# Kernel optimization log

Hardware: AMD Instinct MI355X
Metric: run time of the kernel (lower is better)

## Reference

```python
import jax, jax.numpy as jnp
import numpy as np

B, S, D = 4, 2048, 1024
H, DK, DV = 16, 64, 64
EPS = 1e-5


def setup_inputs() -> dict:
    key = jax.random.key(0)
    ks = jax.random.split(key, 12)
    sc = 0.02
    return {
        "q": jax.random.normal(ks[0], (B, S, D), jnp.float32),
        "k": jax.random.normal(ks[1], (B, S, D), jnp.float32),
        "v": jax.random.normal(ks[2], (B, S, D), jnp.float32),
        "Wq": jax.random.normal(ks[3], (D, H * DK), jnp.float32) * sc,
        "bq": jnp.zeros((H * DK,), jnp.float32),
        "Wk": jax.random.normal(ks[4], (D, H * DK), jnp.float32) * sc,
        "bk": jnp.zeros((H * DK,), jnp.float32),
        "Wv": jax.random.normal(ks[5], (D, H * DV), jnp.float32) * sc,
        "bv": jnp.zeros((H * DV,), jnp.float32),
        "Wfc": jax.random.normal(ks[6], (H * DV, D), jnp.float32) * sc,
        "bfc": jnp.zeros((D,), jnp.float32),
        "gamma": jnp.ones((D,), jnp.float32),
        "beta": jnp.zeros((D,), jnp.float32),
    }


def _forward(q, k, v, Wq, bq, Wk, bk, Wv, bv, Wfc, bfc, gamma, beta):
    qp = q @ Wq + bq                      # [B,S,H*DK]
    kp = k @ Wk + bk
    vp = v @ Wv + bv
    qh = qp.reshape(B, S, H, DK).transpose(0, 2, 1, 3)  # [B,H,S,DK]
    kh = kp.reshape(B, S, H, DK).transpose(0, 2, 1, 3)
    vh = vp.reshape(B, S, H, DV).transpose(0, 2, 1, 3)
    scores = jnp.einsum("bhqd,bhkd->bhqk", qh, kh) / jnp.sqrt(jnp.float32(DK))
    attn = jax.nn.softmax(scores, axis=-1)
    ctx = jnp.einsum("bhqk,bhkd->bhqd", attn, vh)       # [B,H,S,DV]
    ctx = ctx.transpose(0, 2, 1, 3).reshape(B, S, H * DV)
    out = ctx @ Wfc + bfc                 # [B,S,D]
    residual = qp                         # n_heads*d_k == d_model
    x = out + residual
    mu = jnp.mean(x, axis=-1, keepdims=True)
    var = jnp.mean((x - mu) ** 2, axis=-1, keepdims=True)
    return (x - mu) / jnp.sqrt(var + EPS) * gamma + beta


def reference(q, k, v, Wq, bq, Wk, bk, Wv, bv, Wfc, bfc, gamma, beta):
    return _forward(q, k, v, Wq, bq, Wk, bk, Wv, bv, Wfc, bfc, gamma, beta)
```

## Files before the change

### kernel.cpp

```cpp
#include <hip/hip_runtime.h>
#include <hip/hip_bf16.h>
#include <stdint.h>

typedef __bf16 bf16x8 __attribute__((ext_vector_type(8)));
typedef __bf16 bf16x4 __attribute__((ext_vector_type(4)));
typedef short  s16x4  __attribute__((ext_vector_type(4)));
typedef float  f32x4  __attribute__((ext_vector_type(4)));

#define MFMA_K32(a,b,c) __builtin_amdgcn_mfma_f32_16x16x32_bf16((a),(b),(c),0,0,0)

__device__ __forceinline__ f32x4 pv_mfma(s16x4 a, s16x4 b, f32x4 c) {
#if defined(__HIP_DEVICE_COMPILE__)
    return __builtin_amdgcn_mfma_f32_16x16x16bf16_1k(a, b, c, 0, 0, 0);
#else
    return c;
#endif
}

__device__ __forceinline__ void gld16(const void* g, void* l) {
#if defined(__HIP_DEVICE_COMPILE__)
    __builtin_amdgcn_global_load_lds((__attribute__((address_space(1))) void*)(g),
                                     (__attribute__((address_space(3))) void*)(l), 16, 0, 0);
#endif
}

#define CS 0.180336880111f

__global__ __launch_bounds__(256) void cast3_kernel(const float* __restrict__ q,
                                                    const float* __restrict__ k,
                                                    const float* __restrict__ v,
                                                    __hip_bfloat16* __restrict__ qb,
                                                    __hip_bfloat16* __restrict__ kb,
                                                    __hip_bfloat16* __restrict__ vb) {
    const float* x = (blockIdx.y == 0) ? q : (blockIdx.y == 1) ? k : v;
    __hip_bfloat16* y = (blockIdx.y == 0) ? qb : (blockIdx.y == 1) ? kb : vb;
    int i = blockIdx.x * 256 + threadIdx.x;
    float4 vv = ((const float4*)x)[i];
    union { ushort4 u; __hip_bfloat16 b[4]; } c;
    c.b[0] = __float2bfloat16(vv.x);
    c.b[1] = __float2bfloat16(vv.y);
    c.b[2] = __float2bfloat16(vv.z);
    c.b[3] = __float2bfloat16(vv.w);
    ((ushort4*)y)[i] = c.u;
}

__global__ __launch_bounds__(256) void transpose_w_kernel(const float* __restrict__ Wq,
                                                          const float* __restrict__ Wk,
                                                          const float* __restrict__ Wv,
                                                          const float* __restrict__ Wfc,
                                                          __hip_bfloat16* __restrict__ WqT,
                                                          __hip_bfloat16* __restrict__ WkT,
                                                          __hip_bfloat16* __restrict__ WvT,
                                                          __hip_bfloat16* __restrict__ WfcT) {
    int z = blockIdx.z;
    const float* W = (z == 0) ? Wq : (z == 1) ? Wk : (z == 2) ? Wv : Wfc;
    __hip_bfloat16* Wt = (z == 0) ? WqT : (z == 1) ? WkT : (z == 2) ? WvT : WfcT;
    __shared__ float tile[32][33];
    int n0 = blockIdx.x * 32, k0 = blockIdx.y * 32;
    int tx = threadIdx.x & 31, ty = threadIdx.x >> 5;
    for (int i = ty; i < 32; i += 8)
        tile[i][tx] = W[(size_t)(k0 + i) * 1024 + n0 + tx];
    __syncthreads();
    for (int i = ty; i < 32; i += 8)
        Wt[(size_t)(n0 + i) * 1024 + k0 + tx] = __float2bfloat16(tile[tx][i]);
}

__global__ __launch_bounds__(256) void transpose_v_kernel(const __hip_bfloat16* __restrict__ vp,
                                                          __hip_bfloat16* __restrict__ vt) {
    __shared__ __hip_bfloat16 tile[64][65];
    int s0 = blockIdx.x * 64;
    int bh = blockIdx.y; int bb = bh >> 4, h = bh & 15;
    int tx = threadIdx.x & 63, ty = threadIdx.x >> 6;
    for (int i = ty; i < 64; i += 4)
        tile[i][tx] = vp[(size_t)(bb * 2048 + s0 + i) * 1024 + h * 64 + tx];
    __syncthreads();
    for (int i = ty; i < 64; i += 4)
        vt[((size_t)bh * 64 + i) * 2048 + s0 + tx] = tile[tx][i];
}

__global__ __launch_bounds__(256) void gemm_qkv_kernel(const __hip_bfloat16* __restrict__ qb,
                                                       const __hip_bfloat16* __restrict__ kb,
                                                       const __hip_bfloat16* __restrict__ vb,
                                                       const __hip_bfloat16* __restrict__ WqT,
                                                       const __hip_bfloat16* __restrict__ WkT,
                                                       const __hip_bfloat16* __restrict__ WvT,
                                                       const float* __restrict__ bq,
                                                       const float* __restrict__ bk,
                                                       const float* __restrict__ bv,
                                                       __hip_bfloat16* __restrict__ qp,
                                                       __hip_bfloat16* __restrict__ kp,
                                                       __hip_bfloat16* __restrict__ vp) {
    __shared__ __attribute__((aligned(16))) __hip_bfloat16 As[2][128 * 32];
    __shared__ __attribute__((aligned(16))) __hip_bfloat16 Bs[2][128 * 32];
    const int t = threadIdx.x;
    const int lane = t & 63, w = t >> 6;
    const int m16 = lane & 15, quad = lane >> 4;
    const int wm = w >> 1, wn = w & 1;
    const int sel = blockIdx.y >> 3;
    const int bn = blockIdx.y & 7, bm = blockIdx.x;

    const __hip_bfloat16* A;  const __hip_bfloat16* Bt;
    const float* bias;        __hip_bfloat16* out;
    float oscale = 1.0f;
    if (sel == 0)      { A = qb; Bt = WqT; bias = bq; out = qp; }
    else if (sel == 1) { A = kb; Bt = WkT; bias = bk; out = kp; oscale = CS; }
    else               { A = vb; Bt = WvT; bias = bv; out = vp; }

    const __hip_bfloat16* Ag = A + (size_t)(bm * 128 + (t >> 2)) * 1024 + (t & 3) * 8;
    const __hip_bfloat16* Bg = Bt + (size_t)(bn * 128 + (t >> 2)) * 1024 + (t & 3) * 8;

    auto stage = [&](int k0, int buf) {
        gld16(Ag + k0,                    &As[buf][t * 8]);
        gld16(Ag + (size_t)64 * 1024 + k0, &As[buf][2048 + t * 8]);
        gld16(Bg + k0,                    &Bs[buf][t * 8]);
        gld16(Bg + (size_t)64 * 1024 + k0, &Bs[buf][2048 + t * 8]);
    };

    f32x4 acc[4][4] = {};
    stage(0, 0);

    for (int k0 = 0; k0 < 1024; k0 += 32) {
        const int buf = (k0 >> 5) & 1;
        __syncthreads();
        if (k0 + 32 < 1024) stage(k0 + 32, buf ^ 1);
        bf16x8 af[4], bfr[4];
#pragma unroll
        for (int i = 0; i < 4; ++i) {
            af[i]  = *(const bf16x8*)&As[buf][(wm * 64 + i * 16 + m16) * 32 + quad * 8];
            bfr[i] = *(const bf16x8*)&Bs[buf][(wn * 64 + i * 16 + m16) * 32 + quad * 8];
        }
#pragma unroll
        for (int i = 0; i < 4; ++i)
#pragma unroll
            for (int j = 0; j < 4; ++j)
                acc[i][j] = MFMA_K32(af[i], bfr[j], acc[i][j]);
    }

#pragma unroll
    for (int j = 0; j < 4; ++j) {
        int col = bn * 128 + wn * 64 + j * 16 + m16;
        float bv_ = bias[col];
#pragma unroll
        for (int i = 0; i < 4; ++i) {
            int row0 = bm * 128 + wm * 64 + i * 16 + quad * 4;
#pragma unroll
            for (int r = 0; r < 4; ++r)
                out[(size_t)(row0 + r) * 1024 + col] = __float2bfloat16((acc[i][j][r] + bv_) * oscale);
        }
    }
}

__global__ __launch_bounds__(256) void gemm_fc_kernel(const __hip_bfloat16* __restrict__ A,
                                                      const __hip_bfloat16* __restrict__ Bt,
                                                      const float* __restrict__ bias,
                                                      const __hip_bfloat16* __restrict__ res,
                                                      float* __restrict__ Cf) {
    __shared__ __attribute__((aligned(16))) __hip_bfloat16 As[2][64 * 32];
    __shared__ __attribute__((aligned(16))) __hip_bfloat16 Bs[2][128 * 32];
    const int t = threadIdx.x;
    const int lane = t & 63, w = t >> 6;
    const int m16 = lane & 15, quad = lane >> 4;
    const int bm = blockIdx.x, bn = blockIdx.y;

    const __hip_bfloat16* Ag = A + (size_t)(bm * 64 + (t >> 2)) * 1024 + (t & 3) * 8;
    const __hip_bfloat16* Bg = Bt + (size_t)(bn * 128 + (t >> 2)) * 1024 + (t & 3) * 8;

    auto stage = [&](int k0, int buf) {
        gld16(Ag + k0,                     &As[buf][t * 8]);
        gld16(Bg + k0,                     &Bs[buf][t * 8]);
        gld16(Bg + (size_t)64 * 1024 + k0, &Bs[buf][2048 + t * 8]);
    };

    f32x4 acc[4][2] = {};
    stage(0, 0);

    for (int k0 = 0; k0 < 1024; k0 += 32) {
        const int buf = (k0 >> 5) & 1;
        __syncthreads();
        if (k0 + 32 < 1024) stage(k0 + 32, buf ^ 1);
        bf16x8 af[4], bfr[2];
#pragma unroll
        for (int i = 0; i < 4; ++i)
            af[i] = *(const bf16x8*)&As[buf][(i * 16 + m16) * 32 + quad * 8];
#pragma unroll
        for (int j = 0; j < 2; ++j)
            bfr[j] = *(const bf16x8*)&Bs[buf][(w * 32 + j * 16 + m16) * 32 + quad * 8];
#pragma unroll
        for (int i = 0; i < 4; ++i)
#pragma unroll
            for (int j = 0; j < 2; ++j)
                acc[i][j] = MFMA_K32(af[i], bfr[j], acc[i][j]);
    }

#pragma unroll
    for (int j = 0; j < 2; ++j) {
        int col = bn * 128 + w * 32 + j * 16 + m16;
        float bv_ = bias[col];
#pragma unroll
        for (int i = 0; i < 4; ++i) {
            int row0 = bm * 64 + i * 16 + quad * 4;
#pragma unroll
            for (int r = 0; r < 4; ++r) {
                size_t idx = (size_t)(row0 + r) * 1024 + col;
                Cf[idx] = acc[i][j][r] + bv_ + __bfloat162float(res[idx]);
            }
        }
    }
}

__global__ __launch_bounds__(256, 2) void attn_kernel(const __hip_bfloat16* __restrict__ qp,
                                                      const __hip_bfloat16* __restrict__ kp,
                                                      const __hip_bfloat16* __restrict__ vt,
                                                      __hip_bfloat16* __restrict__ ctx) {
    __shared__ __attribute__((aligned(16))) __hip_bfloat16 Ks[2][128 * 64];
    __shared__ __attribute__((aligned(16))) __hip_bfloat16 Vs[2][64 * 136];

    const int t = threadIdx.x;
    const int lane = t & 63, w = t >> 6;
    const int m16 = lane & 15, quad = lane >> 4;
    const int qtile = blockIdx.x >> 3;
    const int bh = (blockIdx.x & 7) + 8 * blockIdx.y;
    const int b = bh >> 4, h = bh & 15;

    const __hip_bfloat16* qbase = qp + (size_t)(b * 2048 + qtile * 128 + w * 32) * 1024 + h * 64;
    bf16x8 qf[2][2];
#pragma unroll
    for (int nt = 0; nt < 2; ++nt)
#pragma unroll
        for (int ks = 0; ks < 2; ++ks)
            qf[nt][ks] = *(const bf16x8*)(qbase + (size_t)(nt * 16 + m16) * 1024 + ks * 32 + quad * 8);

    const __hip_bfloat16* kg_ = kp + (size_t)(b * 2048) * 1024 + h * 64;
    const __hip_bfloat16* vg_ = vt + (size_t)bh * 64 * 2048;

    auto stageK = [&](int kt, int buf) {
#pragma unroll
        for (int i = 0; i < 4; ++i) {
            int key = kt * 128 + (i & 1) * 64 + (t >> 2);
            gld16(kg_ + (size_t)key * 1024 + (i >> 1) * 32 + (t & 3) * 8, &Ks[buf][i * 2048 + t * 8]);
        }
    };
    bf16x8 vreg[4];
    auto loadV = [&](int kt) {
#pragma unroll
        for (int i = 0; i < 4; ++i)
            vreg[i] = *(const bf16x8*)(vg_ + (size_t)(i * 16 + (t >> 4)) * 2048 + kt * 128 + (t & 15) * 8);
    };
    auto writeV = [&](int buf) {
#pragma unroll
        for (int i = 0; i < 4; ++i)
            *(bf16x8*)&Vs[buf][(i * 16 + (t >> 4)) * 136 + (t & 15) * 8] = vreg[i];
    };

    f32x4 oacc[4][2] = {};
    f32x4 lsv[2] = {};

    stageK(0, 0);
    loadV(0);

    for (int kt = 0; kt < 16; ++kt) {
        const int buf = kt & 1;
        writeV(buf);
        __syncthreads();
        if (kt + 1 < 16) { stageK(kt + 1, buf ^ 1); loadV(kt + 1); }

        f32x4 sacc[8][2] = {};
#pragma unroll
        for (int ks = 0; ks < 2; ++ks)
#pragma unroll
            for (int mt = 0; mt < 8; ++mt) {
                bf16x8 kf = *(const bf16x8*)&Ks[buf][ks * 4096 + (mt * 16 + m16) * 32 + quad * 8];
                sacc[mt][0] = MFMA_K32(kf, qf[0][ks], sacc[mt][0]);
                sacc[mt][1] = MFMA_K32(kf, qf[1][ks], sacc[mt][1]);
            }

        s16x4 pf[8][2];
#pragma unroll
        for (int mt = 0; mt < 8; ++mt)
#pragma unroll
            for (int nt = 0; nt < 2; ++nt) {
                union { s16x4 s; __bf16 bb[4]; } up;
#pragma unroll
                for (int r = 0; r < 4; ++r) {
                    float pv = __builtin_amdgcn_exp2f(sacc[mt][nt][r]);
                    lsv[nt][r] += pv;
                    up.bb[r] = (__bf16)pv;
                }
                pf[mt][nt] = up.s;
            }

#pragma unroll
        for (int dt = 0; dt < 4; ++dt)
#pragma unroll
            for (int ks2 = 0; ks2 < 8; ++ks2) {
                bf16x4 vfb = *(const bf16x4*)&Vs[buf][(dt * 16 + m16) * 136 + ks2 * 16 + quad * 4];
                s16x4 vf = __builtin_bit_cast(s16x4, vfb);
                oacc[dt][0] = pv_mfma(vf, pf[ks2][0], oacc[dt][0]);
                oacc[dt][1] = pv_mfma(vf, pf[ks2][1], oacc[dt][1]);
            }
    }

    float inv[2];
#pragma unroll
    for (int nt = 0; nt < 2; ++nt) {
        float l = lsv[nt][0] + lsv[nt][1] + lsv[nt][2] + lsv[nt][3];
        l += __shfl_xor(l, 16);
        l += __shfl_xor(l, 32);
        inv[nt] = __builtin_amdgcn_rcpf(l);
    }
#pragma unroll
    for (int nt = 0; nt < 2; ++nt) {
        size_t token = (size_t)b * 2048 + qtile * 128 + w * 32 + nt * 16 + m16;
#pragma unroll
        for (int dt = 0; dt < 4; ++dt) {
            union { bf16x4 v; __bf16 bb[4]; } uo;
#pragma unroll
            for (int r = 0; r < 4; ++r)
                uo.bb[r] = (__bf16)(oacc[dt][nt][r] * inv[nt]);
            *(bf16x4*)(ctx + token * 1024 + h * 64 + dt * 16 + quad * 4) = uo.v;
        }
    }
}

__global__ __launch_bounds__(256) void layernorm_kernel(const float* __restrict__ x,
                                                        const float* __restrict__ gamma,
                                                        const float* __restrict__ beta,
                                                        float* __restrict__ out) {
    int row = blockIdx.x;
    int t = threadIdx.x;
    const float4* xr = (const float4*)(x + (size_t)row * 1024);
    float4 v = xr[t];
    float s  = v.x + v.y + v.z + v.w;
    float s2 = v.x * v.x + v.y * v.y + v.z * v.z + v.w * v.w;
#pragma unroll
    for (int off = 32; off > 0; off >>= 1) {
        s  += __shfl_down(s, off);
        s2 += __shfl_down(s2, off);
    }
    __shared__ float red[8];
    int w = t >> 6, lane = t & 63;
    if (lane == 0) { red[w] = s; red[4 + w] = s2; }
    __syncthreads();
    s  = red[0] + red[1] + red[2] + red[3];
    s2 = red[4] + red[5] + red[6] + red[7];
    float mu  = s * (1.f / 1024.f);
    float var = s2 * (1.f / 1024.f) - mu * mu;
    float rstd = rsqrtf(var + 1e-5f);
    float4 g  = ((const float4*)gamma)[t];
    float4 be = ((const float4*)beta)[t];
    float4 o;
    o.x = (v.x - mu) * rstd * g.x + be.x;
    o.y = (v.y - mu) * rstd * g.y + be.y;
    o.z = (v.z - mu) * rstd * g.z + be.z;
    o.w = (v.w - mu) * rstd * g.w + be.w;
    ((float4*)(out + (size_t)row * 1024))[t] = o;
}

extern "C" void kernel_launch(void* const* d_in, const int* in_sizes, int n_in,
                              void* d_out, int out_size, void* d_ws, size_t ws_size,
                              hipStream_t stream) {
    const float* q    = (const float*)d_in[0];
    const float* k    = (const float*)d_in[1];
    const float* v    = (const float*)d_in[2];
    const float* Wq   = (const float*)d_in[3];
    const float* bq   = (const float*)d_in[4];
    const float* Wk   = (const float*)d_in[5];
    const float* bk   = (const float*)d_in[6];
    const float* Wv   = (const float*)d_in[7];
    const float* bv   = (const float*)d_in[8];
    const float* Wfc  = (const float*)d_in[9];
    const float* bfc  = (const float*)d_in[10];
    const float* gamma= (const float*)d_in[11];
    const float* beta = (const float*)d_in[12];
    float* out = (float*)d_out;

    char* ws = (char*)d_ws;
    const size_t SZ  = (size_t)8192 * 1024 * 2;
    const size_t WSZ = (size_t)1024 * 1024 * 2;
    __hip_bfloat16* qb  = (__hip_bfloat16*)(ws + 0 * SZ);
    __hip_bfloat16* kb  = (__hip_bfloat16*)(ws + 1 * SZ);
    __hip_bfloat16* vb  = (__hip_bfloat16*)(ws + 2 * SZ);
    __hip_bfloat16* qp  = (__hip_bfloat16*)(ws + 3 * SZ);
    __hip_bfloat16* kp  = (__hip_bfloat16*)(ws + 4 * SZ);
    __hip_bfloat16* vp  = (__hip_bfloat16*)(ws + 5 * SZ);
    __hip_bfloat16* ctx = (__hip_bfloat16*)(ws + 6 * SZ);
    __hip_bfloat16* WqT = (__hip_bfloat16*)(ws + 7 * SZ);
    __hip_bfloat16* WkT = (__hip_bfloat16*)(ws + 7 * SZ + 1 * WSZ);
    __hip_bfloat16* WvT = (__hip_bfloat16*)(ws + 7 * SZ + 2 * WSZ);
    __hip_bfloat16* WfcT= (__hip_bfloat16*)(ws + 7 * SZ + 3 * WSZ);
    float*          x   = (float*)(ws + 0 * SZ);
    __hip_bfloat16* vt  = vb;

    cast3_kernel<<<dim3(8192, 3), 256, 0, stream>>>(q, k, v, qb, kb, vb);

    transpose_w_kernel<<<dim3(32, 32, 4), 256, 0, stream>>>(Wq, Wk, Wv, Wfc, WqT, WkT, WvT, WfcT);

    gemm_qkv_kernel<<<dim3(64, 24), 256, 0, stream>>>(qb, kb, vb, WqT, WkT, WvT,
                                                      bq, bk, bv, qp, kp, vp);

    transpose_v_kernel<<<dim3(32, 64), 256, 0, stream>>>(vp, vt);

    attn_kernel<<<dim3(128, 8), 256, 0, stream>>>(qp, kp, vt, ctx);

    gemm_fc_kernel<<<dim3(128, 8), 256, 0, stream>>>(ctx, WfcT, bfc, qp, x);

    layernorm_kernel<<<8192, 256, 0, stream>>>(x, gamma, beta, out);
}
```

Before: 376.0 us.

## Fuse input cast into QKV GEMM, enlarge FC tile, use MFMA for softmax row sums

The separate fp32-to-bf16 cast kernel is removed. The QKV GEMM now loads fp32 activations into registers, packs them to bf16 with a cheap rounding perm and stores them into LDS, overlapping this with the MFMAs. That saves a full write and re-read of three 32 MB tensors. The FC GEMM moves from 64x128 to 128x128 tiles (half the grid). The attention kernel packs P with a faster bf16 conversion, reorders the PV loop, and computes row sums with an extra MFMA against a ones vector instead of scalar adds and shuffles. Costs: register pressure from the held fp32 A tile, and rounding that differs slightly from round-to-nearest-even (no NaN handling).

```diff
diff --git a/kernel.cpp b/kernel.cpp
--- a/kernel.cpp
+++ b/kernel.cpp
@@ -24,25 +24,17 @@
 #endif
 }
 
+__device__ __forceinline__ uint32_t pkbf16(float f0, float f1) {
+    uint32_t u0 = __builtin_bit_cast(uint32_t, f0) + 0x8000u;
+    uint32_t u1 = __builtin_bit_cast(uint32_t, f1) + 0x8000u;
+#if defined(__HIP_DEVICE_COMPILE__)
+    return __builtin_amdgcn_perm(u1, u0, 0x07060302u);
+#else
+    return (u0 >> 16) | (u1 & 0xFFFF0000u);
+#endif
+}
+
 #define CS 0.180336880111f
-
-__global__ __launch_bounds__(256) void cast3_kernel(const float* __restrict__ q,
-                                                    const float* __restrict__ k,
-                                                    const float* __restrict__ v,
-                                                    __hip_bfloat16* __restrict__ qb,
-                                                    __hip_bfloat16* __restrict__ kb,
-                                                    __hip_bfloat16* __restrict__ vb) {
-    const float* x = (blockIdx.y == 0) ? q : (blockIdx.y == 1) ? k : v;
-    __hip_bfloat16* y = (blockIdx.y == 0) ? qb : (blockIdx.y == 1) ? kb : vb;
-    int i = blockIdx.x * 256 + threadIdx.x;
-    float4 vv = ((const float4*)x)[i];
-    union { ushort4 u; __hip_bfloat16 b[4]; } c;
-    c.b[0] = __float2bfloat16(vv.x);
-    c.b[1] = __float2bfloat16(vv.y);
-    c.b[2] = __float2bfloat16(vv.z);
-    c.b[3] = __float2bfloat16(vv.w);
-    ((ushort4*)y)[i] = c.u;
-}
 
 __global__ __launch_bounds__(256) void transpose_w_kernel(const float* __restrict__ Wq,
                                                           const float* __restrict__ Wk,
@@ -78,9 +70,9 @@
         vt[((size_t)bh * 64 + i) * 2048 + s0 + tx] = tile[tx][i];
 }
 
-__global__ __launch_bounds__(256) void gemm_qkv_kernel(const __hip_bfloat16* __restrict__ qb,
-                                                       const __hip_bfloat16* __restrict__ kb,
-                                                       const __hip_bfloat16* __restrict__ vb,
+__global__ __launch_bounds__(256) void gemm_qkv_kernel(const float* __restrict__ q,
+                                                       const float* __restrict__ k,
+                                                       const float* __restrict__ v,
                                                        const __hip_bfloat16* __restrict__ WqT,
                                                        const __hip_bfloat16* __restrict__ WkT,
                                                        const __hip_bfloat16* __restrict__ WvT,
@@ -99,20 +91,96 @@
     const int sel = blockIdx.y >> 3;
     const int bn = blockIdx.y & 7, bm = blockIdx.x;
 
-    const __hip_bfloat16* A;  const __hip_bfloat16* Bt;
-    const float* bias;        __hip_bfloat16* out;
+    const float* A;  const __hip_bfloat16* Bt;
+    const float* bias;  __hip_bfloat16* out;
     float oscale = 1.0f;
-    if (sel == 0)      { A = qb; Bt = WqT; bias = bq; out = qp; }
-    else if (sel == 1) { A = kb; Bt = WkT; bias = bk; out = kp; oscale = CS; }
-    else               { A = vb; Bt = WvT; bias = bv; out = vp; }
+    if (sel == 0)      { A = q; Bt = WqT; bias = bq; out = qp; }
+    else if (sel == 1) { A = k; Bt = WkT; bias = bk; out = kp; oscale = CS; }
+    else               { A = v; Bt = WvT; bias = bv; out = vp; }
+
+    const float* Ag = A + (size_t)(bm * 128 + (t >> 2)) * 1024 + (t & 3) * 8;
+    const __hip_bfloat16* Bg = Bt + (size_t)(bn * 128 + (t >> 2)) * 1024 + (t & 3) * 8;
+
+    auto stageB = [&](int k0, int buf) {
+        gld16(Bg + k0,                     &Bs[buf][t * 8]);
+        gld16(Bg + (size_t)64 * 1024 + k0, &Bs[buf][2048 + t * 8]);
+    };
+    float4 fA[4];
+    auto loadA = [&](int k0) {
+        const float4* p0 = (const float4*)(Ag + k0);
+        const float4* p1 = (const float4*)(Ag + (size_t)64 * 1024 + k0);
+        fA[0] = p0[0]; fA[1] = p0[1];
+        fA[2] = p1[0]; fA[3] = p1[1];
+    };
+    auto packA = [&](int buf) {
+#pragma unroll
+        for (int p = 0; p < 2; ++p) {
+            uint4 wv;
+            wv.x = pkbf16(fA[2 * p].x,     fA[2 * p].y);
+            wv.y = pkbf16(fA[2 * p].z,     fA[2 * p].w);
+            wv.z = pkbf16(fA[2 * p + 1].x, fA[2 * p + 1].y);
+            wv.w = pkbf16(fA[2 * p + 1].z, fA[2 * p + 1].w);
+            *(uint4*)&As[buf][p * 2048 + t * 8] = wv;
+        }
+    };
+
+    f32x4 acc[4][4] = {};
+    loadA(0);
+    stageB(0, 0);
+    packA(0);
+
+    for (int k0 = 0; k0 < 1024; k0 += 32) {
+        const int buf = (k0 >> 5) & 1;
+        __syncthreads();
+        if (k0 + 32 < 1024) { loadA(k0 + 32); stageB(k0 + 32, buf ^ 1); }
+        bf16x8 af[4], bfr[4];
+#pragma unroll
+        for (int i = 0; i < 4; ++i) {
+            af[i]  = *(const bf16x8*)&As[buf][(wm * 64 + i * 16 + m16) * 32 + quad * 8];
+            bfr[i] = *(const bf16x8*)&Bs[buf][(wn * 64 + i * 16 + m16) * 32 + quad * 8];
+        }
+#pragma unroll
+        for (int i = 0; i < 4; ++i)
+#pragma unroll
+            for (int j = 0; j < 4; ++j)
+                acc[i][j] = MFMA_K32(af[i], bfr[j], acc[i][j]);
+        if (k0 + 32 < 1024) packA(buf ^ 1);
+    }
+
+#pragma unroll
+    for (int j = 0; j < 4; ++j) {
+        int col = bn * 128 + wn * 64 + j * 16 + m16;
+        float bv_ = bias[col];
+#pragma unroll
+        for (int i = 0; i < 4; ++i) {
+            int row0 = bm * 128 + wm * 64 + i * 16 + quad * 4;
+#pragma unroll
+            for (int r = 0; r < 4; ++r)
+                out[(size_t)(row0 + r) * 1024 + col] = __float2bfloat16((acc[i][j][r] + bv_) * oscale);
+        }
+    }
+}
+
+__global__ __launch_bounds__(256) void gemm_fc_kernel(const __hip_bfloat16* __restrict__ A,
+                                                      const __hip_bfloat16* __restrict__ Bt,
+                                                      const float* __restrict__ bias,
+                                                      const __hip_bfloat16* __restrict__ res,
+                                                      float* __restrict__ Cf) {
+    __shared__ __attribute__((aligned(16))) __hip_bfloat16 As[2][128 * 32];
+    __shared__ __attribute__((aligned(16))) __hip_bfloat16 Bs[2][128 * 32];
+    const int t = threadIdx.x;
+    const int lane = t & 63, w = t >> 6;
+    const int m16 = lane & 15, quad = lane >> 4;
+    const int wm = w >> 1, wn = w & 1;
+    const int bm = blockIdx.x, bn = blockIdx.y;
 
     const __hip_bfloat16* Ag = A + (size_t)(bm * 128 + (t >> 2)) * 1024 + (t & 3) * 8;
     const __hip_bfloat16* Bg = Bt + (size_t)(bn * 128 + (t >> 2)) * 1024 + (t & 3) * 8;
 
     auto stage = [&](int k0, int buf) {
-        gld16(Ag + k0,                    &As[buf][t * 8]);
+        gld16(Ag + k0,                     &As[buf][t * 8]);
         gld16(Ag + (size_t)64 * 1024 + k0, &As[buf][2048 + t * 8]);
-        gld16(Bg + k0,                    &Bs[buf][t * 8]);
+        gld16(Bg + k0,                     &Bs[buf][t * 8]);
         gld16(Bg + (size_t)64 * 1024 + k0, &Bs[buf][2048 + t * 8]);
     };
 
@@ -143,62 +211,6 @@
 #pragma unroll
         for (int i = 0; i < 4; ++i) {
             int row0 = bm * 128 + wm * 64 + i * 16 + quad * 4;
-#pragma unroll
-            for (int r = 0; r < 4; ++r)
-                out[(size_t)(row0 + r) * 1024 + col] = __float2bfloat16((acc[i][j][r] + bv_) * oscale);
-        }
-    }
-}
-
-__global__ __launch_bounds__(256) void gemm_fc_kernel(const __hip_bfloat16* __restrict__ A,
-                                                      const __hip_bfloat16* __restrict__ Bt,
-                                                      const float* __restrict__ bias,
-                                                      const __hip_bfloat16* __restrict__ res,
-                                                      float* __restrict__ Cf) {
-    __shared__ __attribute__((aligned(16))) __hip_bfloat16 As[2][64 * 32];
-    __shared__ __attribute__((aligned(16))) __hip_bfloat16 Bs[2][128 * 32];
-    const int t = threadIdx.x;
-    const int lane = t & 63, w = t >> 6;
-    const int m16 = lane & 15, quad = lane >> 4;
-    const int bm = blockIdx.x, bn = blockIdx.y;
-
-    const __hip_bfloat16* Ag = A + (size_t)(bm * 64 + (t >> 2)) * 1024 + (t & 3) * 8;
-    const __hip_bfloat16* Bg = Bt + (size_t)(bn * 128 + (t >> 2)) * 1024 + (t & 3) * 8;
-
-    auto stage = [&](int k0, int buf) {
-        gld16(Ag + k0,                     &As[buf][t * 8]);
-        gld16(Bg + k0,                     &Bs[buf][t * 8]);
-        gld16(Bg + (size_t)64 * 1024 + k0, &Bs[buf][2048 + t * 8]);
-    };
-
-    f32x4 acc[4][2] = {};
-    stage(0, 0);
-
-    for (int k0 = 0; k0 < 1024; k0 += 32) {
-        const int buf = (k0 >> 5) & 1;
-        __syncthreads();
-        if (k0 + 32 < 1024) stage(k0 + 32, buf ^ 1);
-        bf16x8 af[4], bfr[2];
-#pragma unroll
-        for (int i = 0; i < 4; ++i)
-            af[i] = *(const bf16x8*)&As[buf][(i * 16 + m16) * 32 + quad * 8];
-#pragma unroll
-        for (int j = 0; j < 2; ++j)
-            bfr[j] = *(const bf16x8*)&Bs[buf][(w * 32 + j * 16 + m16) * 32 + quad * 8];
-#pragma unroll
-        for (int i = 0; i < 4; ++i)
-#pragma unroll
-            for (int j = 0; j < 2; ++j)
-                acc[i][j] = MFMA_K32(af[i], bfr[j], acc[i][j]);
-    }
-
-#pragma unroll
-    for (int j = 0; j < 2; ++j) {
-        int col = bn * 128 + w * 32 + j * 16 + m16;
-        float bv_ = bias[col];
-#pragma unroll
-        for (int i = 0; i < 4; ++i) {
-            int row0 = bm * 64 + i * 16 + quad * 4;
 #pragma unroll
             for (int r = 0; r < 4; ++r) {
                 size_t idx = (size_t)(row0 + r) * 1024 + col;
@@ -253,7 +265,8 @@
     };
 
     f32x4 oacc[4][2] = {};
-    f32x4 lsv[2] = {};
+    f32x4 lacc[2] = {};
+    const s16x4 ones = {0x3F80, 0x3F80, 0x3F80, 0x3F80};
 
     stageK(0, 0);
     loadV(0);
@@ -279,35 +292,34 @@
         for (int mt = 0; mt < 8; ++mt)
 #pragma unroll
             for (int nt = 0; nt < 2; ++nt) {
-                union { s16x4 s; __bf16 bb[4]; } up;
-#pragma unroll
-                for (int r = 0; r < 4; ++r) {
-                    float pv = __builtin_amdgcn_exp2f(sacc[mt][nt][r]);
-                    lsv[nt][r] += pv;
-                    up.bb[r] = (__bf16)pv;
-                }
-                pf[mt][nt] = up.s;
+                float p0 = __builtin_amdgcn_exp2f(sacc[mt][nt][0]);
+                float p1 = __builtin_amdgcn_exp2f(sacc[mt][nt][1]);
+                float p2 = __builtin_amdgcn_exp2f(sacc[mt][nt][2]);
+                float p3 = __builtin_amdgcn_exp2f(sacc[mt][nt][3]);
+                uint2 wv;
+                wv.x = pkbf16(p0, p1);
+                wv.y = pkbf16(p2, p3);
+                pf[mt][nt] = __builtin_bit_cast(s16x4, wv);
             }
 
 #pragma unroll
-        for (int dt = 0; dt < 4; ++dt)
-#pragma unroll
-            for (int ks2 = 0; ks2 < 8; ++ks2) {
+        for (int ks2 = 0; ks2 < 8; ++ks2) {
+#pragma unroll
+            for (int dt = 0; dt < 4; ++dt) {
                 bf16x4 vfb = *(const bf16x4*)&Vs[buf][(dt * 16 + m16) * 136 + ks2 * 16 + quad * 4];
                 s16x4 vf = __builtin_bit_cast(s16x4, vfb);
                 oacc[dt][0] = pv_mfma(vf, pf[ks2][0], oacc[dt][0]);
                 oacc[dt][1] = pv_mfma(vf, pf[ks2][1], oacc[dt][1]);
             }
+            lacc[0] = pv_mfma(ones, pf[ks2][0], lacc[0]);
+            lacc[1] = pv_mfma(ones, pf[ks2][1], lacc[1]);
+        }
     }
 
     float inv[2];
 #pragma unroll
-    for (int nt = 0; nt < 2; ++nt) {
-        float l = lsv[nt][0] + lsv[nt][1] + lsv[nt][2] + lsv[nt][3];
-        l += __shfl_xor(l, 16);
-        l += __shfl_xor(l, 32);
-        inv[nt] = __builtin_amdgcn_rcpf(l);
-    }
+    for (int nt = 0; nt < 2; ++nt)
+        inv[nt] = __builtin_amdgcn_rcpf(lacc[nt][0]);
 #pragma unroll
     for (int nt = 0; nt < 2; ++nt) {
         size_t token = (size_t)b * 2048 + qtile * 128 + w * 32 + nt * 16 + m16;
@@ -377,9 +389,8 @@
     char* ws = (char*)d_ws;
     const size_t SZ  = (size_t)8192 * 1024 * 2;
     const size_t WSZ = (size_t)1024 * 1024 * 2;
-    __hip_bfloat16* qb  = (__hip_bfloat16*)(ws + 0 * SZ);
-    __hip_bfloat16* kb  = (__hip_bfloat16*)(ws + 1 * SZ);
-    __hip_bfloat16* vb  = (__hip_bfloat16*)(ws + 2 * SZ);
+    float*          x   = (float*)(ws + 0 * SZ);
+    __hip_bfloat16* vt  = (__hip_bfloat16*)(ws + 2 * SZ);
     __hip_bfloat16* qp  = (__hip_bfloat16*)(ws + 3 * SZ);
     __hip_bfloat16* kp  = (__hip_bfloat16*)(ws + 4 * SZ);
     __hip_bfloat16* vp  = (__hip_bfloat16*)(ws + 5 * SZ);
@@ -388,21 +399,17 @@
     __hip_bfloat16* WkT = (__hip_bfloat16*)(ws + 7 * SZ + 1 * WSZ);
     __hip_bfloat16* WvT = (__hip_bfloat16*)(ws + 7 * SZ + 2 * WSZ);
     __hip_bfloat16* WfcT= (__hip_bfloat16*)(ws + 7 * SZ + 3 * WSZ);
-    float*          x   = (float*)(ws + 0 * SZ);
-    __hip_bfloat16* vt  = vb;
-
-    cast3_kernel<<<dim3(8192, 3), 256, 0, stream>>>(q, k, v, qb, kb, vb);
 
     transpose_w_kernel<<<dim3(32, 32, 4), 256, 0, stream>>>(Wq, Wk, Wv, Wfc, WqT, WkT, WvT, WfcT);
 
-    gemm_qkv_kernel<<<dim3(64, 24), 256, 0, stream>>>(qb, kb, vb, WqT, WkT, WvT,
+    gemm_qkv_kernel<<<dim3(64, 24), 256, 0, stream>>>(q, k, v, WqT, WkT, WvT,
                                                       bq, bk, bv, qp, kp, vp);
 
     transpose_v_kernel<<<dim3(32, 64), 256, 0, stream>>>(vp, vt);
 
     attn_kernel<<<dim3(128, 8), 256, 0, stream>>>(qp, kp, vt, ctx);
 
-    gemm_fc_kernel<<<dim3(128, 8), 256, 0, stream>>>(ctx, WfcT, bfc, qp, x);
+    gemm_fc_kernel<<<dim3(64, 8), 256, 0, stream>>>(ctx, WfcT, bfc, qp, x);
 
     layernorm_kernel<<<8192, 256, 0, stream>>>(x, gamma, beta, out);
 }
```

New measurement: 439.3 us. 16.9% more time.
